# Kernel optimization log

Hardware: AMD Instinct MI355X
Metric: run time of the kernel (lower is better)

Reference implementation:

```python
import jax, jax.numpy as jnp
import numpy as np

VOCAB, EMBED, HIDDEN = 32000, 256, 64
B, T = 4096, 64


def setup_inputs() -> dict:
    key = jax.random.key(0)
    ks = jax.random.split(key, 6)
    s = 1.0 / float(np.sqrt(HIDDEN))  # PyTorch LSTM init scale
    x = jax.random.randint(ks[0], (B, T), 0, VOCAB)
    embed_table = jax.random.normal(ks[1], (VOCAB, EMBED), jnp.float32)
    W_ih = jax.random.uniform(ks[2], (4 * HIDDEN, EMBED), jnp.float32, -s, s)
    W_hh = jax.random.uniform(ks[3], (4 * HIDDEN, HIDDEN), jnp.float32, -s, s)
    b_ih = jax.random.uniform(ks[4], (4 * HIDDEN,), jnp.float32, -s, s)
    b_hh = jax.random.uniform(ks[5], (4 * HIDDEN,), jnp.float32, -s, s)
    return {"x": x, "embed_table": embed_table, "W_ih": W_ih, "W_hh": W_hh, "b_ih": b_ih, "b_hh": b_hh}


def reference(x, embed_table, W_ih, W_hh, b_ih, b_hh):
    # Embedding lookup: [B,T,E]
    emb = embed_table[x]
    # Precompute input projection for all timesteps (PyTorch gate order i,f,g,o)
    xg = jnp.einsum('bte,ge->btg', emb, W_ih) + (b_ih + b_hh)  # [B,T,4H]
    xg = jnp.swapaxes(xg, 0, 1)  # [T,B,4H]
    h0 = jnp.zeros((x.shape[0], HIDDEN), xg.dtype)
    c0 = jnp.zeros((x.shape[0], HIDDEN), xg.dtype)

    def step(carry, xt):
        h, c = carry
        g = xt + h @ W_hh.T  # [B,4H]
        i, f, gg, o = jnp.split(g, 4, axis=-1)
        c = jax.nn.sigmoid(f) * c + jax.nn.sigmoid(i) * jnp.tanh(gg)
        h = jax.nn.sigmoid(o) * jnp.tanh(c)
        return (h, c), None

    (h, _), _ = jax.lax.scan(step, (h0, c0), xg)
    return h  # [B, HIDDEN] == hidden.squeeze(0)
```

## Files before the change

kernel.cpp:

```cpp
#include <hip/hip_runtime.h>
#include <math.h>

#define B_ 4096
#define T_ 64
#define E_ 256
#define H_ 64
#define V_ 32000
#define THREADS 768

typedef __attribute__((ext_vector_type(8))) short bf16x8;
typedef __attribute__((ext_vector_type(4))) float f32x4;
typedef __attribute__((ext_vector_type(4))) unsigned int u32x4;

__device__ __forceinline__ short f2bf(float x) {
    unsigned u = __float_as_uint(x);
    return (short)((u + 0x7FFFu + ((u >> 16) & 1u)) >> 16);
}
__device__ __forceinline__ unsigned cvt_pk_bf16(float lo, float hi) {
    unsigned r;
    asm("v_cvt_pk_bf16_f32 %0, %1, %2" : "=v"(r) : "v"(lo), "v"(hi));
    return r;
}
__device__ __forceinline__ float exp2_raw(float x) {
    float r; asm("v_exp_f32 %0, %1" : "=v"(r) : "v"(x)); return r;
}
__device__ __forceinline__ float rcp_raw(float x) {
    float r; asm("v_rcp_f32 %0, %1" : "=v"(r) : "v"(x)); return r;
}
#define LOG2E 1.442695041f

template <int CTRL>
__device__ __forceinline__ float dpp_f(float x) {
    return __int_as_float(
        __builtin_amdgcn_mov_dpp(__float_as_int(x), CTRL, 0xF, 0xF, true));
}

__device__ __forceinline__ void gld16(const void* g, void* l) {
    __builtin_amdgcn_global_load_lds(
        (const __attribute__((address_space(1))) void*)g,
        (__attribute__((address_space(3))) void*)l, 16, 0, 0);
}

__global__ void prep_kernel(const float* __restrict__ W_ih,
                            const float* __restrict__ W_hh,
                            const float* __restrict__ b_ih,
                            const float* __restrict__ b_hh,
                            const float* __restrict__ emb_table,
                            short* __restrict__ wih_frag,
                            short* __restrict__ whh_g,
                            float* __restrict__ bias_f,
                            short* __restrict__ emb_bf,
                            int tabN) {
    int tid = blockIdx.x * blockDim.x + threadIdx.x;
    int stride = gridDim.x * blockDim.x;
    for (int i = tid; i < 65536; i += stride) {
        int jj = i & 7;
        int l  = (i >> 3) & 63;
        int kc = (i >> 9) & 7;
        int tl = (i >> 12) & 1;
        int vv = i >> 13;
        int uu = (l & 15) >> 1, pp = l & 1;
        int g = tl * 128 + pp * 64 + vv * 8 + uu;
        int k = kc * 32 + (l >> 4) * 8 + jj;
        wih_frag[i] = f2bf(W_ih[g * E_ + k]);
    }
    for (int i = tid; i < 256 * 64; i += stride) whh_g[i] = f2bf(W_hh[i]);
    for (int i = tid; i < 256; i += stride) bias_f[i] = b_ih[i] + b_hh[i];
    for (int i = tid; i < (tabN >> 3); i += stride) {
        float4 v0 = ((const float4*)emb_table)[i * 2];
        float4 v1 = ((const float4*)emb_table)[i * 2 + 1];
        u32x4 w;
        w[0] = cvt_pk_bf16(v0.x, v0.y);
        w[1] = cvt_pk_bf16(v0.z, v0.w);
        w[2] = cvt_pk_bf16(v1.x, v1.y);
        w[3] = cvt_pk_bf16(v1.z, v1.w);
        ((u32x4*)emb_bf)[i] = w;
    }
}

template <int TAB>
__global__ __attribute__((amdgpu_flat_work_group_size(THREADS, THREADS),
                          amdgpu_waves_per_eu(3, 3)))
void lstm_f(const int* __restrict__ x,
            const float* __restrict__ embf,
            const short* __restrict__ embb,
            const short* __restrict__ wih_frag,
            const short* __restrict__ whh_g,
            const float* __restrict__ bias_f,
            float* __restrict__ out) {
    __shared__ __align__(16) short s_ef[4][4096];
    __shared__ __align__(16) short s_hf[2][1024];
    __shared__ int s_idx[1024];

    const int tid  = threadIdx.x;
    const int lane = tid & 63;
    const int wave = tid >> 6;
    const int r0   = blockIdx.x * 16;

    for (int i = tid; i < 1024; i += THREADS)
        s_idx[(i & 63) * 16 + (i >> 6)] = x[(r0 + (i >> 6)) * T_ + (i & 63)];
    for (int i = tid; i < 1024; i += THREADS)
        ((int*)s_hf)[i] = 0;

    const int p  = lane & 1;
    const int c4 = lane >> 4;
    const int u  = (lane & 15) >> 1;
    const float scl2 = p ? 1.0f : 2.0f;
    const float offB = p ? 0.0f : -1.0f;
    const float enB  = -LOG2E * scl2;
    const int m0 = c4 * 4 + p * 2;

    bf16x8 wA[8], wB[8], qA0, qA1, qB0, qB1;
    float bA = 0.f, bB = 0.f;
    int hw_s = 0;
    if (wave < 8) {
        const short* wp = wih_frag + wave * 8192 + lane * 8;
        #pragma unroll
        for (int kc = 0; kc < 8; ++kc) {
            wA[kc] = *(const bf16x8*)(wp + kc * 512);
            wB[kc] = *(const bf16x8*)(wp + 4096 + kc * 512);
        }
        const int gA = p * 64 + wave * 8 + u;
        const short* qp = whh_g + gA * 64 + c4 * 8;
        qA0 = *(const bf16x8*)(qp);
        qA1 = *(const bf16x8*)(qp + 32);
        qB0 = *(const bf16x8*)(qp + 8192);
        qB1 = *(const bf16x8*)(qp + 8192 + 32);
        bA = bias_f[gA];
        bB = bias_f[gA + 128];
        hw_s = (wave >> 2) * 512 + (wave & 3) * 128
             + ((u & 1) ? (m0 + 1) * 8 + (u - 1) : m0 * 8 + u);
    }

    const int m16    = lane & 15;
    const int kc0    = (wave - 8) * 2;
    const int sbase0 = kc0 * 512 + lane * 8;
    const int skoff0 = kc0 * 32 + (lane >> 4) * 8;
    const int skoff1 = skoff0 + 32;

    __syncthreads();

    if (wave >= 8) {
        #pragma unroll
        for (int tt = 0; tt < 3; ++tt) {
            int tok = s_idx[tt * 16 + m16];
            if (TAB) {
                gld16(embb + (size_t)tok * E_ + skoff0, &s_ef[tt][kc0 * 512]);
                gld16(embb + (size_t)tok * E_ + skoff1, &s_ef[tt][kc0 * 512 + 512]);
            } else {
                const float* pr = embf + (size_t)tok * E_;
                #pragma unroll
                for (int kk = 0; kk < 2; ++kk) {
                    const float* q = pr + skoff0 + kk * 32;
                    float4 f0 = *(const float4*)q;
                    float4 f1 = *(const float4*)(q + 4);
                    u32x4 w;
                    w[0] = cvt_pk_bf16(f0.x, f0.y);
                    w[1] = cvt_pk_bf16(f0.z, f0.w);
                    w[2] = cvt_pk_bf16(f1.x, f1.y);
                    w[3] = cvt_pk_bf16(f1.z, f1.w);
                    *(u32x4*)(&s_ef[tt][0] + sbase0 + kk * 512) = w;
                }
            }
        }
    }
    if (TAB) {
        asm volatile("s_waitcnt vmcnt(2) lgkmcnt(0)" ::: "memory");
        __builtin_amdgcn_s_barrier();
        __builtin_amdgcn_sched_barrier(0);
    } else {
        __syncthreads();
    }

    float c0 = 0.f, c1 = 0.f, h0v = 0.f, h1v = 0.f;
    f32x4 a0, a1, b0, b1;

    if (wave < 8) {
        a0 = (f32x4){bA, bA, bA, bA};
        b0 = (f32x4){bB, bB, bB, bB};
        a1 = (f32x4){0.f, 0.f, 0.f, 0.f};
        b1 = (f32x4){0.f, 0.f, 0.f, 0.f};
        const short* eb = &s_ef[0][0] + lane * 8;
        #pragma unroll
        for (int kc = 0; kc < 4; ++kc) {
            bf16x8 av = *(const bf16x8*)(eb + kc * 512);
            bf16x8 aw = *(const bf16x8*)(eb + (kc + 4) * 512);
            a0 = __builtin_amdgcn_mfma_f32_16x16x32_bf16(av, wA[kc], a0, 0, 0, 0);
            b0 = __builtin_amdgcn_mfma_f32_16x16x32_bf16(av, wB[kc], b0, 0, 0, 0);
            a1 = __builtin_amdgcn_mfma_f32_16x16x32_bf16(aw, wA[kc + 4], a1, 0, 0, 0);
            b1 = __builtin_amdgcn_mfma_f32_16x16x32_bf16(aw, wB[kc + 4], b1, 0, 0, 0);
        }
    }

    auto gates_phase = [&](const float* ga, const float* gb, int t) {
        float sA[4], Bv[4];
        #pragma unroll
        for (int q = 0; q < 4; ++q) {
            sA[q] = rcp_raw(1.0f + exp2_raw(-LOG2E * ga[q]));
            Bv[q] = rcp_raw(1.0f + exp2_raw(enB * gb[q])) * scl2 + offB;
        }
        float s1 = p ? sA[0] : sA[2] * Bv[2];
        float r1 = dpp_f<0xB1>(s1);
        float s2 = p ? sA[1] : sA[3] * Bv[3];
        float r2 = dpp_f<0xB1>(s2);
        float r3 = dpp_f<0xB1>(Bv[0]);
        float r4 = dpp_f<0xB1>(Bv[1]);
        float fc0 = p ? sA[2] : r1;
        float ic0 = p ? r1 : sA[0] * Bv[0];
        float oc0 = p ? Bv[2] : r3;
        float fc1 = p ? sA[3] : r2;
        float ic1 = p ? r2 : sA[1] * Bv[1];
        float oc1 = p ? Bv[3] : r4;
        c0 = fc0 * c0 + ic0;
        c1 = fc1 * c1 + ic1;
        h0v = oc0 * (1.0f - 2.0f * rcp_raw(1.0f + exp2_raw(2.0f * LOG2E * c0)));
        h1v = oc1 * (1.0f - 2.0f * rcp_raw(1.0f + exp2_raw(2.0f * LOG2E * c1)));
        float snd = (u & 1) ? h0v : h1v;
        float rcv = dpp_f<0x4E>(snd);
        unsigned hw = (u & 1) ? cvt_pk_bf16(rcv, h1v) : cvt_pk_bf16(h0v, rcv);
        *(unsigned*)(&s_hf[(t + 1) & 1][0] + hw_s) = hw;
    };

    auto p_phase = [&](int t) {
        a0 = (f32x4){bA, bA, bA, bA};
        b0 = (f32x4){bB, bB, bB, bB};
        a1 = (f32x4){0.f, 0.f, 0.f, 0.f};
        b1 = (f32x4){0.f, 0.f, 0.f, 0.f};
        const short* eb = &s_ef[(t + 1) & 3][0] + lane * 8;
        __builtin_amdgcn_s_setprio(1);
        #pragma unroll
        for (int kc = 0; kc < 4; ++kc) {
            bf16x8 av = *(const bf16x8*)(eb + kc * 512);
            bf16x8 aw = *(const bf16x8*)(eb + (kc + 4) * 512);
            a0 = __builtin_amdgcn_mfma_f32_16x16x32_bf16(av, wA[kc], a0, 0, 0, 0);
            b0 = __builtin_amdgcn_mfma_f32_16x16x32_bf16(av, wB[kc], b0, 0, 0, 0);
            a1 = __builtin_amdgcn_mfma_f32_16x16x32_bf16(aw, wA[kc + 4], a1, 0, 0, 0);
            b1 = __builtin_amdgcn_mfma_f32_16x16x32_bf16(aw, wB[kc + 4], b1, 0, 0, 0);
        }
        __builtin_amdgcn_s_setprio(0);
    };

    #pragma unroll 4
    for (int t = 0; t < T_; ++t) {
        if (wave < 8) {
            const short* hb = &s_hf[t & 1][0] + lane * 8;
            bf16x8 hv0 = *(const bf16x8*)(hb);
            bf16x8 hv1 = *(const bf16x8*)(hb + 512);
            __builtin_amdgcn_s_setprio(1);
            a0 = __builtin_amdgcn_mfma_f32_16x16x32_bf16(hv0, qA0, a0, 0, 0, 0);
            a1 = __builtin_amdgcn_mfma_f32_16x16x32_bf16(hv1, qA1, a1, 0, 0, 0);
            b0 = __builtin_amdgcn_mfma_f32_16x16x32_bf16(hv0, qB0, b0, 0, 0, 0);
            b1 = __builtin_amdgcn_mfma_f32_16x16x32_bf16(hv1, qB1, b1, 0, 0, 0);
            __builtin_amdgcn_s_setprio(0);

            float ga[4], gb[4];
            #pragma unroll
            for (int q = 0; q < 4; ++q) {
                ga[q] = a0[q] + a1[q];
                gb[q] = b0[q] + b1[q];
            }

            if (wave < 4) {
                gates_phase(ga, gb, t);
                if (t < T_ - 1) p_phase(t);
            } else {
                __builtin_amdgcn_sched_barrier(0);
                if (t < T_ - 1) p_phase(t);
                __builtin_amdgcn_sched_barrier(0);
                gates_phase(ga, gb, t);
            }
        } else {
            if (t + 3 < T_) {
                int tok = s_idx[(t + 3) * 16 + m16];
                if (TAB) {
                    gld16(embb + (size_t)tok * E_ + skoff0,
                          &s_ef[(t + 3) & 3][kc0 * 512]);
                    gld16(embb + (size_t)tok * E_ + skoff1,
                          &s_ef[(t + 3) & 3][kc0 * 512 + 512]);
                } else {
                    const float* pr = embf + (size_t)tok * E_;
                    #pragma unroll
                    for (int kk = 0; kk < 2; ++kk) {
                        const float* q = pr + skoff0 + kk * 32;
                        float4 f0 = *(const float4*)q;
                        float4 f1 = *(const float4*)(q + 4);
                        u32x4 w;
                        w[0] = cvt_pk_bf16(f0.x, f0.y);
                        w[1] = cvt_pk_bf16(f0.z, f0.w);
                        w[2] = cvt_pk_bf16(f1.x, f1.y);
                        w[3] = cvt_pk_bf16(f1.z, f1.w);
                        *(u32x4*)(&s_ef[(t + 3) & 3][0] + sbase0 + kk * 512) = w;
                    }
                }
            }
        }
        if (TAB) {
            asm volatile("s_waitcnt vmcnt(2) lgkmcnt(0)" ::: "memory");
            __builtin_amdgcn_s_barrier();
            __builtin_amdgcn_sched_barrier(0);
        } else {
            __syncthreads();
        }
    }

    if (wave < 8) {
        const int j = wave * 8 + u;
        out[(r0 + m0) * H_ + j]     = h0v;
        out[(r0 + m0 + 1) * H_ + j] = h1v;
    }
}

extern "C" void kernel_launch(void* const* d_in, const int* in_sizes, int n_in,
                              void* d_out, int out_size, void* d_ws, size_t ws_size,
                              hipStream_t stream) {
    const int*   x         = (const int*)d_in[0];
    const float* emb_table = (const float*)d_in[1];
    const float* W_ih      = (const float*)d_in[2];
    const float* W_hh      = (const float*)d_in[3];
    const float* b_ih      = (const float*)d_in[4];
    const float* b_hh      = (const float*)d_in[5];
    float*       out       = (float*)d_out;

    short* wih_frag = (short*)d_ws;
    short* whh_g    = wih_frag + 65536;
    float* bias_f   = (float*)(whh_g + 16384);
    short* emb_bf   = (short*)(bias_f + 256);

    const size_t need = (size_t)(65536 + 16384) * 2 + 256 * 4
                      + (size_t)V_ * E_ * 2;
    const int tab = (ws_size >= need) ? 1 : 0;

    prep_kernel<<<tab ? 2048 : 64, 256, 0, stream>>>(
        W_ih, W_hh, b_ih, b_hh, emb_table,
        wih_frag, whh_g, bias_f,
        tab ? emb_bf : wih_frag, tab ? V_ * E_ : 0);

    if (tab) {
        lstm_f<1><<<B_ / 16, THREADS, 0, stream>>>(
            x, emb_table, emb_bf, wih_frag, whh_g, bias_f, out);
    } else {
        lstm_f<0><<<B_ / 16, THREADS, 0, stream>>>(
            x, emb_table, wih_frag, wih_frag, whh_g, bias_f, out);
    }
}
```

Baseline: 63.33 us.

## Drop prep kernel; convert weights and embeddings to bf16 inside LSTM kernel

Removes the separate prep kernel that pre-converted W_ih/W_hh into bf16 fragment layouts and converted the whole embedding table to bf16. The main kernel now reads fp32 weights directly, packs them to bf16 in registers, sums the biases itself, and always gathers fp32 embedding rows with in-kernel conversion. This avoids a launch and a full-table conversion pass over 32000x256 floats. In exchange it gives up the async global_load_lds path and the split waitcnt barrier, doubles gathered embedding bytes per step, and adds strided per-block weight loads.

```diff
diff --git a/kernel.cpp b/kernel.cpp
--- a/kernel.cpp
+++ b/kernel.cpp
@@ -5,17 +5,12 @@
 #define T_ 64
 #define E_ 256
 #define H_ 64
-#define V_ 32000
 #define THREADS 768
 
 typedef __attribute__((ext_vector_type(8))) short bf16x8;
 typedef __attribute__((ext_vector_type(4))) float f32x4;
 typedef __attribute__((ext_vector_type(4))) unsigned int u32x4;
 
-__device__ __forceinline__ short f2bf(float x) {
-    unsigned u = __float_as_uint(x);
-    return (short)((u + 0x7FFFu + ((u >> 16) & 1u)) >> 16);
-}
 __device__ __forceinline__ unsigned cvt_pk_bf16(float lo, float hi) {
     unsigned r;
     asm("v_cvt_pk_bf16_f32 %0, %1, %2" : "=v"(r) : "v"(lo), "v"(hi));
@@ -35,58 +30,27 @@
         __builtin_amdgcn_mov_dpp(__float_as_int(x), CTRL, 0xF, 0xF, true));
 }
 
-__device__ __forceinline__ void gld16(const void* g, void* l) {
-    __builtin_amdgcn_global_load_lds(
-        (const __attribute__((address_space(1))) void*)g,
-        (__attribute__((address_space(3))) void*)l, 16, 0, 0);
-}
-
-__global__ void prep_kernel(const float* __restrict__ W_ih,
-                            const float* __restrict__ W_hh,
-                            const float* __restrict__ b_ih,
-                            const float* __restrict__ b_hh,
-                            const float* __restrict__ emb_table,
-                            short* __restrict__ wih_frag,
-                            short* __restrict__ whh_g,
-                            float* __restrict__ bias_f,
-                            short* __restrict__ emb_bf,
-                            int tabN) {
-    int tid = blockIdx.x * blockDim.x + threadIdx.x;
-    int stride = gridDim.x * blockDim.x;
-    for (int i = tid; i < 65536; i += stride) {
-        int jj = i & 7;
-        int l  = (i >> 3) & 63;
-        int kc = (i >> 9) & 7;
-        int tl = (i >> 12) & 1;
-        int vv = i >> 13;
-        int uu = (l & 15) >> 1, pp = l & 1;
-        int g = tl * 128 + pp * 64 + vv * 8 + uu;
-        int k = kc * 32 + (l >> 4) * 8 + jj;
-        wih_frag[i] = f2bf(W_ih[g * E_ + k]);
-    }
-    for (int i = tid; i < 256 * 64; i += stride) whh_g[i] = f2bf(W_hh[i]);
-    for (int i = tid; i < 256; i += stride) bias_f[i] = b_ih[i] + b_hh[i];
-    for (int i = tid; i < (tabN >> 3); i += stride) {
-        float4 v0 = ((const float4*)emb_table)[i * 2];
-        float4 v1 = ((const float4*)emb_table)[i * 2 + 1];
-        u32x4 w;
-        w[0] = cvt_pk_bf16(v0.x, v0.y);
-        w[1] = cvt_pk_bf16(v0.z, v0.w);
-        w[2] = cvt_pk_bf16(v1.x, v1.y);
-        w[3] = cvt_pk_bf16(v1.z, v1.w);
-        ((u32x4*)emb_bf)[i] = w;
-    }
-}
-
-template <int TAB>
+__device__ __forceinline__ bf16x8 pack8(const float* q) {
+    float4 f0 = *(const float4*)q;
+    float4 f1 = *(const float4*)(q + 4);
+    u32x4 w;
+    w[0] = cvt_pk_bf16(f0.x, f0.y);
+    w[1] = cvt_pk_bf16(f0.z, f0.w);
+    w[2] = cvt_pk_bf16(f1.x, f1.y);
+    w[3] = cvt_pk_bf16(f1.z, f1.w);
+    union { u32x4 u; bf16x8 s; } cvt;
+    cvt.u = w;
+    return cvt.s;
+}
+
 __global__ __attribute__((amdgpu_flat_work_group_size(THREADS, THREADS),
                           amdgpu_waves_per_eu(3, 3)))
-void lstm_f(const int* __restrict__ x,
-            const float* __restrict__ embf,
-            const short* __restrict__ embb,
-            const short* __restrict__ wih_frag,
-            const short* __restrict__ whh_g,
-            const float* __restrict__ bias_f,
+void lstm_k(const int* __restrict__ x,
+            const float* __restrict__ emb,
+            const float* __restrict__ W_ih,
+            const float* __restrict__ W_hh,
+            const float* __restrict__ b_ih,
+            const float* __restrict__ b_hh,
             float* __restrict__ out) {
     __shared__ __align__(16) short s_ef[4][4096];
     __shared__ __align__(16) short s_hf[2][1024];
@@ -114,20 +78,22 @@
     float bA = 0.f, bB = 0.f;
     int hw_s = 0;
     if (wave < 8) {
-        const short* wp = wih_frag + wave * 8192 + lane * 8;
+        const int gA = p * 64 + wave * 8 + u;
+        const float* wi0 = W_ih + (size_t)gA * E_;
+        const float* wi1 = W_ih + (size_t)(128 + gA) * E_;
         #pragma unroll
         for (int kc = 0; kc < 8; ++kc) {
-            wA[kc] = *(const bf16x8*)(wp + kc * 512);
-            wB[kc] = *(const bf16x8*)(wp + 4096 + kc * 512);
-        }
-        const int gA = p * 64 + wave * 8 + u;
-        const short* qp = whh_g + gA * 64 + c4 * 8;
-        qA0 = *(const bf16x8*)(qp);
-        qA1 = *(const bf16x8*)(qp + 32);
-        qB0 = *(const bf16x8*)(qp + 8192);
-        qB1 = *(const bf16x8*)(qp + 8192 + 32);
-        bA = bias_f[gA];
-        bB = bias_f[gA + 128];
+            wA[kc] = pack8(wi0 + kc * 32 + c4 * 8);
+            wB[kc] = pack8(wi1 + kc * 32 + c4 * 8);
+        }
+        const float* qh0 = W_hh + (size_t)gA * H_ + c4 * 8;
+        const float* qh1 = W_hh + (size_t)(128 + gA) * H_ + c4 * 8;
+        qA0 = pack8(qh0);
+        qA1 = pack8(qh0 + 32);
+        qB0 = pack8(qh1);
+        qB1 = pack8(qh1 + 32);
+        bA = b_ih[gA] + b_hh[gA];
+        bB = b_ih[gA + 128] + b_hh[gA + 128];
         hw_s = (wave >> 2) * 512 + (wave & 3) * 128
              + ((u & 1) ? (m0 + 1) * 8 + (u - 1) : m0 * 8 + u);
     }
@@ -136,7 +102,6 @@
     const int kc0    = (wave - 8) * 2;
     const int sbase0 = kc0 * 512 + lane * 8;
     const int skoff0 = kc0 * 32 + (lane >> 4) * 8;
-    const int skoff1 = skoff0 + 32;
 
     __syncthreads();
 
@@ -144,33 +109,22 @@
         #pragma unroll
         for (int tt = 0; tt < 3; ++tt) {
             int tok = s_idx[tt * 16 + m16];
-            if (TAB) {
-                gld16(embb + (size_t)tok * E_ + skoff0, &s_ef[tt][kc0 * 512]);
-                gld16(embb + (size_t)tok * E_ + skoff1, &s_ef[tt][kc0 * 512 + 512]);
-            } else {
-                const float* pr = embf + (size_t)tok * E_;
-                #pragma unroll
-                for (int kk = 0; kk < 2; ++kk) {
-                    const float* q = pr + skoff0 + kk * 32;
-                    float4 f0 = *(const float4*)q;
-                    float4 f1 = *(const float4*)(q + 4);
-                    u32x4 w;
-                    w[0] = cvt_pk_bf16(f0.x, f0.y);
-                    w[1] = cvt_pk_bf16(f0.z, f0.w);
-                    w[2] = cvt_pk_bf16(f1.x, f1.y);
-                    w[3] = cvt_pk_bf16(f1.z, f1.w);
-                    *(u32x4*)(&s_ef[tt][0] + sbase0 + kk * 512) = w;
-                }
-            }
-        }
-    }
-    if (TAB) {
-        asm volatile("s_waitcnt vmcnt(2) lgkmcnt(0)" ::: "memory");
-        __builtin_amdgcn_s_barrier();
-        __builtin_amdgcn_sched_barrier(0);
-    } else {
-        __syncthreads();
-    }
+            const float* pr = emb + (size_t)tok * E_;
+            #pragma unroll
+            for (int kk = 0; kk < 2; ++kk) {
+                const float* q = pr + skoff0 + kk * 32;
+                float4 f0 = *(const float4*)q;
+                float4 f1 = *(const float4*)(q + 4);
+                u32x4 w;
+                w[0] = cvt_pk_bf16(f0.x, f0.y);
+                w[1] = cvt_pk_bf16(f0.z, f0.w);
+                w[2] = cvt_pk_bf16(f1.x, f1.y);
+                w[3] = cvt_pk_bf16(f1.z, f1.w);
+                *(u32x4*)(&s_ef[tt][0] + sbase0 + kk * 512) = w;
+            }
+        }
+    }
+    __syncthreads();
 
     float c0 = 0.f, c1 = 0.f, h0v = 0.f, h1v = 0.f;
     f32x4 a0, a1, b0, b1;
@@ -272,35 +226,22 @@
         } else {
             if (t + 3 < T_) {
                 int tok = s_idx[(t + 3) * 16 + m16];
-                if (TAB) {
-                    gld16(embb + (size_t)tok * E_ + skoff0,
-                          &s_ef[(t + 3) & 3][kc0 * 512]);
-                    gld16(embb + (size_t)tok * E_ + skoff1,
-                          &s_ef[(t + 3) & 3][kc0 * 512 + 512]);
-                } else {
-                    const float* pr = embf + (size_t)tok * E_;
-                    #pragma unroll
-                    for (int kk = 0; kk < 2; ++kk) {
-                        const float* q = pr + skoff0 + kk * 32;
-                        float4 f0 = *(const float4*)q;
-                        float4 f1 = *(const float4*)(q + 4);
-                        u32x4 w;
-                        w[0] = cvt_pk_bf16(f0.x, f0.y);
-                        w[1] = cvt_pk_bf16(f0.z, f0.w);
-                        w[2] = cvt_pk_bf16(f1.x, f1.y);
-                        w[3] = cvt_pk_bf16(f1.z, f1.w);
-                        *(u32x4*)(&s_ef[(t + 3) & 3][0] + sbase0 + kk * 512) = w;
-                    }
+                const float* pr = emb + (size_t)tok * E_;
+                #pragma unroll
+                for (int kk = 0; kk < 2; ++kk) {
+                    const float* q = pr + skoff0 + kk * 32;
+                    float4 f0 = *(const float4*)q;
+                    float4 f1 = *(const float4*)(q + 4);
+                    u32x4 w;
+                    w[0] = cvt_pk_bf16(f0.x, f0.y);
+                    w[1] = cvt_pk_bf16(f0.z, f0.w);
+                    w[2] = cvt_pk_bf16(f1.x, f1.y);
+                    w[3] = cvt_pk_bf16(f1.z, f1.w);
+                    *(u32x4*)(&s_ef[(t + 3) & 3][0] + sbase0 + kk * 512) = w;
                 }
             }
         }
-        if (TAB) {
-            asm volatile("s_waitcnt vmcnt(2) lgkmcnt(0)" ::: "memory");
-            __builtin_amdgcn_s_barrier();
-            __builtin_amdgcn_sched_barrier(0);
-        } else {
-            __syncthreads();
-        }
+        __syncthreads();
     }
 
     if (wave < 8) {
@@ -321,25 +262,6 @@
     const float* b_hh      = (const float*)d_in[5];
     float*       out       = (float*)d_out;
 
-    short* wih_frag = (short*)d_ws;
-    short* whh_g    = wih_frag + 65536;
-    float* bias_f   = (float*)(whh_g + 16384);
-    short* emb_bf   = (short*)(bias_f + 256);
-
-    const size_t need = (size_t)(65536 + 16384) * 2 + 256 * 4
-                      + (size_t)V_ * E_ * 2;
-    const int tab = (ws_size >= need) ? 1 : 0;
-
-    prep_kernel<<<tab ? 2048 : 64, 256, 0, stream>>>(
-        W_ih, W_hh, b_ih, b_hh, emb_table,
-        wih_frag, whh_g, bias_f,
-        tab ? emb_bf : wih_frag, tab ? V_ * E_ : 0);
-
-    if (tab) {
-        lstm_f<1><<<B_ / 16, THREADS, 0, stream>>>(
-            x, emb_table, emb_bf, wih_frag, whh_g, bias_f, out);
-    } else {
-        lstm_f<0><<<B_ / 16, THREADS, 0, stream>>>(
-            x, emb_table, wih_frag, wih_frag, whh_g, bias_f, out);
-    }
-}
+    lstm_k<<<B_ / 16, THREADS, 0, stream>>>(x, emb_table, W_ih, W_hh,
+                                            b_ih, b_hh, out);
+}
```

Result: slower. 75.21 us (+18.8%).
